# Kernel optimization log

Hardware: AMD Instinct MI355X
Metric: run time of the kernel (lower is better)

The kernel has to match this reference:

```python
import jax, jax.numpy as jnp
import numpy as np

N_NODES = 100000
N_EDGES = 1600000
NODE_DIM = 128
HIDDEN_DIM = 128


def _sage_conv(x, src, dst, deg_inv, W_l, W_r, b):
    # PyG SAGEConv (aggr='mean', root_weight=True):
    #   out = lin_l(mean_{j in N(i)} x_j) + lin_r(x_i)
    msgs = x[src]                                             # [E, d_in] gather
    agg = jax.ops.segment_sum(msgs, dst, num_segments=N_NODES)  # [N, d_in]
    mean = agg * deg_inv[:, None]
    return mean @ W_l + x @ W_r + b


def setup_inputs() -> dict:
    key = jax.random.key(0)
    ks = jax.random.split(key, 9)
    x = jax.random.normal(ks[0], (N_NODES, NODE_DIM), dtype=jnp.float32)
    edge_index = jax.random.randint(ks[1], (2, N_EDGES), 0, N_NODES, dtype=jnp.int32)
    t = jnp.zeros((1,), dtype=jnp.float32)

    def glorot(k, fan_in, fan_out):
        s = (6.0 / (fan_in + fan_out)) ** 0.5
        return jax.random.uniform(k, (fan_in, fan_out), jnp.float32, -s, s)

    return {
        "t": t,
        "x": x,
        "edge_index": edge_index,
        "W1_l": glorot(ks[2], NODE_DIM, HIDDEN_DIM),
        "W1_r": glorot(ks[3], NODE_DIM, HIDDEN_DIM),
        "b1": jnp.zeros((HIDDEN_DIM,), jnp.float32),
        "W2_l": glorot(ks[4], HIDDEN_DIM, HIDDEN_DIM),
        "W2_r": glorot(ks[5], HIDDEN_DIM, HIDDEN_DIM),
        "b2": jnp.zeros((HIDDEN_DIM,), jnp.float32),
        "W3_l": glorot(ks[6], HIDDEN_DIM, NODE_DIM),
        "W3_r": glorot(ks[7], HIDDEN_DIM, NODE_DIM),
        "b3": jnp.zeros((NODE_DIM,), jnp.float32),
    }


def reference(t, x, edge_index, W1_l, W1_r, b1, W2_l, W2_r, b2, W3_l, W3_r, b3):
    src, dst = edge_index[0], edge_index[1]
    deg = jax.ops.segment_sum(jnp.ones((N_EDGES,), x.dtype), dst, num_segments=N_NODES)
    deg_inv = jnp.where(deg > 0, 1.0 / jnp.maximum(deg, 1.0), 0.0)

    h = jax.nn.relu(_sage_conv(x, src, dst, deg_inv, W1_l, W1_r, b1))
    h = jax.nn.relu(_sage_conv(h, src, dst, deg_inv, W2_l, W2_r, b2))
    dx_dt = _sage_conv(h, src, dst, deg_inv, W3_l, W3_r, b3)
    return dx_dt
```

## Files before the change

kernel.cpp:

```cpp
#include <hip/hip_runtime.h>

#define NN   100000
#define NE   1600000
#define DIM  128
#define NBKT 391
#define EPB  4096
#define NBLK 391
#define NTILES (NN / 16)
#define CASTB 12500
#define CWB   384


typedef short          s16x8 __attribute__((ext_vector_type(8)));
typedef unsigned short u16x8 __attribute__((ext_vector_type(8)));
typedef float          f32x4 __attribute__((ext_vector_type(4)));

__device__ __forceinline__ unsigned short f2b(float f) {
    unsigned u = __float_as_uint(f);
    unsigned r = ((u >> 16) & 1u) + 0x7FFFu;
    return (unsigned short)((u + r) >> 16);
}
__device__ __forceinline__ float b2f(unsigned short h) {
    return __uint_as_float(((unsigned)h) << 16);
}

__global__ void k_prep(const float* __restrict__ x, unsigned short* __restrict__ xb,
                       const int* __restrict__ dst, int* __restrict__ hist,
                       const float* __restrict__ W1l, const float* __restrict__ W1r,
                       const float* __restrict__ W2l, const float* __restrict__ W2r,
                       const float* __restrict__ W3l, const float* __restrict__ W3r,
                       unsigned short* __restrict__ Wt1, unsigned short* __restrict__ Wt2,
                       unsigned short* __restrict__ Wt3) {
    __shared__ int lh[NBKT];
    int t = threadIdx.x, b = blockIdx.x;
    if (b < NBLK) {
        for (int j = t; j < NBKT; j += 256) lh[j] = 0;
        __syncthreads();
        int base = b * EPB;
        int end = base + EPB; if (end > NE) end = NE;
        for (int i = base + t; i < end; i += 256) atomicAdd(&lh[dst[i] >> 8], 1);
        __syncthreads();
        for (int j = t; j < NBKT; j += 256) hist[j * NBLK + b] = lh[j];
    } else if (b < NBLK + CASTB) {
        int i = (b - NBLK) * 256 + t;
        float4 v = ((const float4*)x)[i];
        ushort4 o;
        o.x = f2b(v.x); o.y = f2b(v.y); o.z = f2b(v.z); o.w = f2b(v.w);
        ((ushort4*)xb)[i] = o;
    } else {
        int i = (b - NBLK - CASTB) * 256 + t;
        int L = i >> 15;
        int rem = i & 32767;
        int n = rem >> 8;
        int k = rem & 255;
        const float* Wl = (L == 0) ? W1l : (L == 1) ? W2l : W3l;
        const float* Wr = (L == 0) ? W1r : (L == 1) ? W2r : W3r;
        unsigned short* Wt = (L == 0) ? Wt1 : (L == 1) ? Wt2 : Wt3;
        float v = (k < 128) ? Wl[k * 128 + n] : Wr[(k - 128) * 128 + n];
        Wt[n * 256 + k] = f2b(v);
    }
}

__global__ void k_scanrow(int* __restrict__ hist, int* __restrict__ row_total) {
    __shared__ int sh[512];
    int k = blockIdx.x, t = threadIdx.x;
    int v = (t < NBLK) ? hist[k * NBLK + t] : 0;
    sh[t] = v;
    __syncthreads();
    for (int off = 1; off < 512; off <<= 1) {
        int a = (t >= off) ? sh[t - off] : 0;
        __syncthreads();
        sh[t] += a;
        __syncthreads();
    }
    if (t < NBLK) hist[k * NBLK + t] = sh[t] - v;
    if (t == 511) row_total[k] = sh[511];
}

__global__ void k_bin2(const int* __restrict__ src, const int* __restrict__ dst,
                       const int* __restrict__ hist, const int* __restrict__ row_total,
                       int* __restrict__ bbase, int* __restrict__ binned) {
    __shared__ int s_base[NBKT];
    __shared__ int s_cnt[NBKT];
    __shared__ int ps[256];
    int t = threadIdx.x, b = blockIdx.x;
    int a0 = (2 * t     < NBKT) ? row_total[2 * t]     : 0;
    int a1 = (2 * t + 1 < NBKT) ? row_total[2 * t + 1] : 0;
    ps[t] = a0 + a1;
    __syncthreads();
    for (int off = 1; off < 256; off <<= 1) {
        int v = (t >= off) ? ps[t - off] : 0;
        __syncthreads();
        ps[t] += v;
        __syncthreads();
    }
    int pe = ps[t] - (a0 + a1);
    if (2 * t     < NBKT) s_base[2 * t]     = pe;
    if (2 * t + 1 < NBKT) s_base[2 * t + 1] = pe + a0;
    __syncthreads();
    if (b == 0) {
        for (int j = t; j < NBKT; j += 256) bbase[j] = s_base[j];
        if (t == 0) bbase[NBKT] = NE;
    }
    for (int j = t; j < NBKT; j += 256) {
        s_base[j] += hist[j * NBLK + b];
        s_cnt[j] = 0;
    }
    __syncthreads();
    int base = b * EPB;
    int end = base + EPB; if (end > NE) end = NE;
    for (int i = base + t; i < end; i += 256) {
        int d = dst[i];
        int k = d >> 8;
        int w = (src[i] << 8) | (d & 255);
        int lpos = atomicAdd(&s_cnt[k], 1);
        binned[s_base[k] + lpos] = w;
    }
}

__global__ void k_build(const int* __restrict__ binned,
                        const int* __restrict__ bucket_base,
                        int* __restrict__ csr, int4* __restrict__ meta) {
    __shared__ int s_deg[256], s_scan[256], s_cur[256];
    __shared__ int stage[8192];
    int b = blockIdx.x, t = threadIdx.x;
    int base = bucket_base[b], end = bucket_base[b + 1];
    int cnt = end - base;
    s_deg[t] = 0;
    __syncthreads();
    for (int i = t; i < cnt; i += 256)
        atomicAdd(&s_deg[binned[base + i] & 255], 1);
    __syncthreads();
    s_scan[t] = s_deg[t];
    __syncthreads();
    for (int off = 1; off < 256; off <<= 1) {
        int a = (t >= off) ? s_scan[t - off] : 0;
        __syncthreads();
        s_scan[t] += a;
        __syncthreads();
    }
    int excl = s_scan[t] - s_deg[t];
    s_cur[t] = excl;
    int node = b * 256 + t;
    if (node < NN) {
        int d = s_deg[t];
        float di = (d > 0) ? 1.0f / (float)d : 0.0f;
        int4 M; M.x = base + excl; M.y = d; M.z = __float_as_int(di); M.w = 0;
        meta[node] = M;
    }
    __syncthreads();
    for (int i = t; i < cnt; i += 256) {
        int w = binned[base + i];
        int pos = atomicAdd(&s_cur[w & 255], 1);
        int s = w >> 8;
        if (pos < 8192) stage[pos] = s;
        else            csr[base + pos] = s;
    }
    __syncthreads();
    int m = cnt < 8192 ? cnt : 8192;
    for (int i = t; i < m; i += 256) csr[base + i] = stage[i];
}

__global__ void k_gather(const unsigned short* __restrict__ feat,
                         const int4* __restrict__ meta,
                         const int* __restrict__ csr,
                         unsigned short* __restrict__ mean) {
    int lane = threadIdx.x & 63;
    int wv   = threadIdx.x >> 6;
    int n    = blockIdx.x * 4 + wv;
    int q = lane >> 4, c = lane & 15;
    int4 M = meta[n];
    int base = M.x;
    int d    = M.y;
    float s  = __int_as_float(M.z);
    float acc0[8], acc1[8];
#pragma unroll
    for (int t = 0; t < 8; t++) { acc0[t] = 0.0f; acc1[t] = 0.0f; }
    const u16x8* fp = (const u16x8*)feat;
    int j = q;
    for (; j + 4 < d; j += 8) {
        int s0 = csr[base + j];
        int s1 = csr[base + j + 4];
        u16x8 v0 = fp[s0 * 16 + c];
        u16x8 v1 = fp[s1 * 16 + c];
#pragma unroll
        for (int t = 0; t < 8; t++) { acc0[t] += b2f(v0[t]); acc1[t] += b2f(v1[t]); }
    }
    if (j < d) {
        int s0 = csr[base + j];
        u16x8 v0 = fp[s0 * 16 + c];
#pragma unroll
        for (int t = 0; t < 8; t++) acc0[t] += b2f(v0[t]);
    }
#pragma unroll
    for (int t = 0; t < 8; t++) acc0[t] += acc1[t];
#pragma unroll
    for (int t = 0; t < 8; t++) {
        acc0[t] += __shfl_xor(acc0[t], 16, 64);
        acc0[t] += __shfl_xor(acc0[t], 32, 64);
    }
    if (q == 0) {
        u16x8 o;
#pragma unroll
        for (int t = 0; t < 8; t++) o[t] = f2b(acc0[t] * s);
        ((u16x8*)mean)[n * 16 + c] = o;
    }
}

template <int MODE>
__global__ void __launch_bounds__(512)
k_lin(const unsigned short* __restrict__ meanb,
      const unsigned short* __restrict__ hb,
      const unsigned short* __restrict__ Wt,
      const float* __restrict__ bias, void* __restrict__ out) {
    __shared__ s16x8 sW[4096];
    int t = threadIdx.x;
    const s16x8* wp = (const s16x8*)Wt;
#pragma unroll
    for (int it = 0; it < 8; it++) {
        int ci = it * 512 + t;
        int frag = ci >> 6, ln = ci & 63;
        int mt = frag >> 3, kt = frag & 7;
        int m = mt * 16 + (ln & 15);
        int kc = kt * 4 + (ln >> 4);
        sW[ci] = wp[m * 32 + kc];
    }
    __syncthreads();

    int lane = t & 63;
    int wv   = t >> 6;
    int tile = blockIdx.x * 8 + wv;
    if (tile >= NTILES) return;
    int n0 = tile * 16;
    int q = lane >> 4, c = lane & 15;
    const s16x8* mp = (const s16x8*)meanb;
    const s16x8* hp = (const s16x8*)hb;
    int row = n0 + c;
    s16x8 B[8];
#pragma unroll
    for (int kt = 0; kt < 4; kt++) B[kt] = mp[row * 16 + kt * 4 + q];
#pragma unroll
    for (int kt = 0; kt < 4; kt++) B[4 + kt] = hp[row * 16 + kt * 4 + q];
    const f32x4* bp = (const f32x4*)bias;
#pragma unroll
    for (int mt = 0; mt < 8; mt++) {
        f32x4 acc = {0.f, 0.f, 0.f, 0.f};
#pragma unroll
        for (int kt = 0; kt < 8; kt++)
            acc = __builtin_amdgcn_mfma_f32_16x16x32_bf16(sW[(mt * 8 + kt) * 64 + lane],
                                                          B[kt], acc, 0, 0, 0);
        f32x4 bv = bp[mt * 4 + q];
        int node = n0 + c;
        if (MODE == 0) {
            ushort4 o;
            float v0 = acc[0] + bv[0]; if (v0 < 0.f) v0 = 0.f;
            float v1 = acc[1] + bv[1]; if (v1 < 0.f) v1 = 0.f;
            float v2 = acc[2] + bv[2]; if (v2 < 0.f) v2 = 0.f;
            float v3 = acc[3] + bv[3]; if (v3 < 0.f) v3 = 0.f;
            o.x = f2b(v0); o.y = f2b(v1); o.z = f2b(v2); o.w = f2b(v3);
            ((ushort4*)out)[node * 32 + mt * 4 + q] = o;
        } else {
            f32x4 v;
#pragma unroll
            for (int r = 0; r < 4; r++) v[r] = acc[r] + bv[r];
            ((f32x4*)out)[node * 32 + mt * 4 + q] = v;
        }
    }
}

extern "C" void kernel_launch(void* const* d_in, const int* in_sizes, int n_in,
                              void* d_out, int out_size, void* d_ws, size_t ws_size,
                              hipStream_t stream) {
    const float* x   = (const float*)d_in[1];
    const int*   ei  = (const int*)d_in[2];
    const int*   src = ei;
    const int*   dst = ei + NE;
    const float* W1l = (const float*)d_in[3];
    const float* W1r = (const float*)d_in[4];
    const float* b1  = (const float*)d_in[5];
    const float* W2l = (const float*)d_in[6];
    const float* W2r = (const float*)d_in[7];
    const float* b2  = (const float*)d_in[8];
    const float* W3l = (const float*)d_in[9];
    const float* W3r = (const float*)d_in[10];
    const float* b3  = (const float*)d_in[11];

    char* w = (char*)d_ws;
    auto carve = [&](size_t bytes) {
        void* p = (void*)w;
        w += (bytes + 255) & ~(size_t)255;
        return p;
    };
    int4*  meta      = (int4*)carve((size_t)NN * 16);
    int*   hist      = (int*)carve((size_t)NBKT * NBLK * 4);
    int*   row_total = (int*)carve(NBKT * 4);
    int*   bbase     = (int*)carve((NBKT + 1) * 4);
    int*   csr       = (int*)carve((size_t)NE * 4);
    unsigned short* Wt1 = (unsigned short*)carve(128 * 256 * 2);
    unsigned short* Wt2 = (unsigned short*)carve(128 * 256 * 2);
    unsigned short* Wt3 = (unsigned short*)carve(128 * 256 * 2);
    unsigned short* xb    = (unsigned short*)carve((size_t)NN * DIM * 2);
    unsigned short* meanb = (unsigned short*)carve((size_t)NN * DIM * 2);
    unsigned short* h1b   = (unsigned short*)carve((size_t)NN * DIM * 2);
    unsigned short* h2b   = xb;
    int*   binned    = (int*)meanb;

    k_prep<<<NBLK + CASTB + CWB, 256, 0, stream>>>(x, xb, dst, hist,
                                                   W1l, W1r, W2l, W2r, W3l, W3r,
                                                   Wt1, Wt2, Wt3);
    k_scanrow<<<NBKT, 512, 0, stream>>>(hist, row_total);
    k_bin2<<<NBLK, 256, 0, stream>>>(src, dst, hist, row_total, bbase, binned);
    k_build<<<NBKT, 256, 0, stream>>>(binned, bbase, csr, meta);

    const int GB = NN / 4;
    const int LB = (NTILES + 7) / 8;

    k_gather<<<GB, 256, 0, stream>>>(xb, meta, csr, meanb);
    k_lin<0><<<LB, 512, 0, stream>>>(meanb, xb, Wt1, b1, (void*)h1b);
    k_gather<<<GB, 256, 0, stream>>>(h1b, meta, csr, meanb);
    k_lin<0><<<LB, 512, 0, stream>>>(meanb, h1b, Wt2, b2, (void*)h2b);
    k_gather<<<GB, 256, 0, stream>>>(h2b, meta, csr, meanb);
    k_lin<1><<<LB, 512, 0, stream>>>(meanb, h2b, Wt3, b3, d_out);
}
```

Before: 417.9 us.

## Replace bucketed CSR build with atomic degree count and scatter; enlarge linear blocks

The two-level bucket histogram, scan, bin and per-bucket build pipeline is replaced by three simple kernels. One counts per-node degree with global atomics, one computes row offsets with a per-block redundant prefix sum, and one scatters sources into CSR via atomic cursors. The bf16 cast now handles two float4 per thread, and the linear kernel uses 1024-thread blocks with activation loads issued before the weight staging. The simpler build drops several launches and passes, but global atomics on contended destinations, a quadratic-ish prefix sum in k_meta, and non-deterministic neighbour order within each row (so float summation order varies) are the trade-offs.

```diff
diff --git a/kernel.cpp b/kernel.cpp
--- a/kernel.cpp
+++ b/kernel.cpp
@@ -3,12 +3,13 @@
 #define NN   100000
 #define NE   1600000
 #define DIM  128
-#define NBKT 391
-#define EPB  4096
-#define NBLK 391
+#define ZB    391
+#define CASTB 6250
+#define CWB   384
+#define EB    6250
 #define NTILES (NN / 16)
-#define CASTB 12500
-#define CWB   384
+#define LB    ((NTILES + 15) / 16)
+#define GB    (NN / 4)
 
 
 typedef short          s16x8 __attribute__((ext_vector_type(8)));
@@ -25,30 +26,27 @@
 }
 
 __global__ void k_prep(const float* __restrict__ x, unsigned short* __restrict__ xb,
-                       const int* __restrict__ dst, int* __restrict__ hist,
+                       int* __restrict__ deg,
                        const float* __restrict__ W1l, const float* __restrict__ W1r,
                        const float* __restrict__ W2l, const float* __restrict__ W2r,
                        const float* __restrict__ W3l, const float* __restrict__ W3r,
                        unsigned short* __restrict__ Wt1, unsigned short* __restrict__ Wt2,
                        unsigned short* __restrict__ Wt3) {
-    __shared__ int lh[NBKT];
     int t = threadIdx.x, b = blockIdx.x;
-    if (b < NBLK) {
-        for (int j = t; j < NBKT; j += 256) lh[j] = 0;
-        __syncthreads();
-        int base = b * EPB;
-        int end = base + EPB; if (end > NE) end = NE;
-        for (int i = base + t; i < end; i += 256) atomicAdd(&lh[dst[i] >> 8], 1);
-        __syncthreads();
-        for (int j = t; j < NBKT; j += 256) hist[j * NBLK + b] = lh[j];
-    } else if (b < NBLK + CASTB) {
-        int i = (b - NBLK) * 256 + t;
-        float4 v = ((const float4*)x)[i];
-        ushort4 o;
-        o.x = f2b(v.x); o.y = f2b(v.y); o.z = f2b(v.z); o.w = f2b(v.w);
-        ((ushort4*)xb)[i] = o;
+    if (b < ZB) {
+        int n = b * 256 + t;
+        if (n < NN) deg[n] = 0;
+    } else if (b < ZB + CASTB) {
+        int i0 = (b - ZB) * 512 + t;
+        float4 v0 = ((const float4*)x)[i0];
+        float4 v1 = ((const float4*)x)[i0 + 256];
+        ushort4 o0, o1;
+        o0.x = f2b(v0.x); o0.y = f2b(v0.y); o0.z = f2b(v0.z); o0.w = f2b(v0.w);
+        o1.x = f2b(v1.x); o1.y = f2b(v1.y); o1.z = f2b(v1.z); o1.w = f2b(v1.w);
+        ((ushort4*)xb)[i0]       = o0;
+        ((ushort4*)xb)[i0 + 256] = o1;
     } else {
-        int i = (b - NBLK - CASTB) * 256 + t;
+        int i = (b - ZB - CASTB) * 256 + t;
         int L = i >> 15;
         int rem = i & 32767;
         int n = rem >> 8;
@@ -61,104 +59,52 @@
     }
 }
 
-__global__ void k_scanrow(int* __restrict__ hist, int* __restrict__ row_total) {
-    __shared__ int sh[512];
-    int k = blockIdx.x, t = threadIdx.x;
-    int v = (t < NBLK) ? hist[k * NBLK + t] : 0;
-    sh[t] = v;
-    __syncthreads();
-    for (int off = 1; off < 512; off <<= 1) {
-        int a = (t >= off) ? sh[t - off] : 0;
-        __syncthreads();
-        sh[t] += a;
-        __syncthreads();
-    }
-    if (t < NBLK) hist[k * NBLK + t] = sh[t] - v;
-    if (t == 511) row_total[k] = sh[511];
-}
-
-__global__ void k_bin2(const int* __restrict__ src, const int* __restrict__ dst,
-                       const int* __restrict__ hist, const int* __restrict__ row_total,
-                       int* __restrict__ bbase, int* __restrict__ binned) {
-    __shared__ int s_base[NBKT];
-    __shared__ int s_cnt[NBKT];
+__global__ void k_degcnt(const int* __restrict__ dst, int* __restrict__ deg) {
+    int i = blockIdx.x * 256 + threadIdx.x;
+    atomicAdd(&deg[dst[i]], 1);
+}
+
+__global__ void k_meta(const int* __restrict__ deg, int4* __restrict__ meta,
+                       int* __restrict__ cursor) {
     __shared__ int ps[256];
     int t = threadIdx.x, b = blockIdx.x;
-    int a0 = (2 * t     < NBKT) ? row_total[2 * t]     : 0;
-    int a1 = (2 * t + 1 < NBKT) ? row_total[2 * t + 1] : 0;
-    ps[t] = a0 + a1;
+    int start = b * 256;
+    int partial = 0;
+    for (int i = t; i < start; i += 256) partial += deg[i];
+    ps[t] = partial;
+    __syncthreads();
+    for (int off = 128; off > 0; off >>= 1) {
+        if (t < off) ps[t] += ps[t + off];
+        __syncthreads();
+    }
+    int S = ps[0];
+    __syncthreads();
+    int n = start + t;
+    int d = (n < NN) ? deg[n] : 0;
+    ps[t] = d;
     __syncthreads();
     for (int off = 1; off < 256; off <<= 1) {
-        int v = (t >= off) ? ps[t - off] : 0;
+        int a = (t >= off) ? ps[t - off] : 0;
         __syncthreads();
-        ps[t] += v;
+        ps[t] += a;
         __syncthreads();
     }
-    int pe = ps[t] - (a0 + a1);
-    if (2 * t     < NBKT) s_base[2 * t]     = pe;
-    if (2 * t + 1 < NBKT) s_base[2 * t + 1] = pe + a0;
-    __syncthreads();
-    if (b == 0) {
-        for (int j = t; j < NBKT; j += 256) bbase[j] = s_base[j];
-        if (t == 0) bbase[NBKT] = NE;
-    }
-    for (int j = t; j < NBKT; j += 256) {
-        s_base[j] += hist[j * NBLK + b];
-        s_cnt[j] = 0;
-    }
-    __syncthreads();
-    int base = b * EPB;
-    int end = base + EPB; if (end > NE) end = NE;
-    for (int i = base + t; i < end; i += 256) {
-        int d = dst[i];
-        int k = d >> 8;
-        int w = (src[i] << 8) | (d & 255);
-        int lpos = atomicAdd(&s_cnt[k], 1);
-        binned[s_base[k] + lpos] = w;
-    }
-}
-
-__global__ void k_build(const int* __restrict__ binned,
-                        const int* __restrict__ bucket_base,
-                        int* __restrict__ csr, int4* __restrict__ meta) {
-    __shared__ int s_deg[256], s_scan[256], s_cur[256];
-    __shared__ int stage[8192];
-    int b = blockIdx.x, t = threadIdx.x;
-    int base = bucket_base[b], end = bucket_base[b + 1];
-    int cnt = end - base;
-    s_deg[t] = 0;
-    __syncthreads();
-    for (int i = t; i < cnt; i += 256)
-        atomicAdd(&s_deg[binned[base + i] & 255], 1);
-    __syncthreads();
-    s_scan[t] = s_deg[t];
-    __syncthreads();
-    for (int off = 1; off < 256; off <<= 1) {
-        int a = (t >= off) ? s_scan[t - off] : 0;
-        __syncthreads();
-        s_scan[t] += a;
-        __syncthreads();
-    }
-    int excl = s_scan[t] - s_deg[t];
-    s_cur[t] = excl;
-    int node = b * 256 + t;
-    if (node < NN) {
-        int d = s_deg[t];
+    int rs = S + (ps[t] - d);
+    if (n < NN) {
         float di = (d > 0) ? 1.0f / (float)d : 0.0f;
-        int4 M; M.x = base + excl; M.y = d; M.z = __float_as_int(di); M.w = 0;
-        meta[node] = M;
-    }
-    __syncthreads();
-    for (int i = t; i < cnt; i += 256) {
-        int w = binned[base + i];
-        int pos = atomicAdd(&s_cur[w & 255], 1);
-        int s = w >> 8;
-        if (pos < 8192) stage[pos] = s;
-        else            csr[base + pos] = s;
-    }
-    __syncthreads();
-    int m = cnt < 8192 ? cnt : 8192;
-    for (int i = t; i < m; i += 256) csr[base + i] = stage[i];
+        int4 M; M.x = rs; M.y = d; M.z = __float_as_int(di); M.w = 0;
+        meta[n]   = M;
+        cursor[n] = rs;
+    }
+}
+
+__global__ void k_scatter(const int* __restrict__ src, const int* __restrict__ dst,
+                          int* __restrict__ cursor, int* __restrict__ csr) {
+    int i = blockIdx.x * 256 + threadIdx.x;
+    int s  = src[i];
+    int d_ = dst[i];
+    int pos = atomicAdd(&cursor[d_], 1);
+    csr[pos] = s;
 }
 
 __global__ void k_gather(const unsigned short* __restrict__ feat,
@@ -208,17 +154,33 @@
 }
 
 template <int MODE>
-__global__ void __launch_bounds__(512)
+__global__ void __launch_bounds__(1024)
 k_lin(const unsigned short* __restrict__ meanb,
       const unsigned short* __restrict__ hb,
       const unsigned short* __restrict__ Wt,
       const float* __restrict__ bias, void* __restrict__ out) {
     __shared__ s16x8 sW[4096];
     int t = threadIdx.x;
+    int lane = t & 63;
+    int wv   = t >> 6;
+    int tile = blockIdx.x * 16 + wv;
+    bool act = (tile < NTILES);
+    int n0 = tile * 16;
+    int q = lane >> 4, c = lane & 15;
+    int row = n0 + c;
+    s16x8 B[8];
+    if (act) {
+        const s16x8* mp = (const s16x8*)meanb;
+        const s16x8* hp = (const s16x8*)hb;
+#pragma unroll
+        for (int kt = 0; kt < 4; kt++) B[kt] = mp[row * 16 + kt * 4 + q];
+#pragma unroll
+        for (int kt = 0; kt < 4; kt++) B[4 + kt] = hp[row * 16 + kt * 4 + q];
+    }
     const s16x8* wp = (const s16x8*)Wt;
 #pragma unroll
-    for (int it = 0; it < 8; it++) {
-        int ci = it * 512 + t;
+    for (int it = 0; it < 4; it++) {
+        int ci = it * 1024 + t;
         int frag = ci >> 6, ln = ci & 63;
         int mt = frag >> 3, kt = frag & 7;
         int m = mt * 16 + (ln & 15);
@@ -226,21 +188,8 @@
         sW[ci] = wp[m * 32 + kc];
     }
     __syncthreads();
-
-    int lane = t & 63;
-    int wv   = t >> 6;
-    int tile = blockIdx.x * 8 + wv;
-    if (tile >= NTILES) return;
-    int n0 = tile * 16;
-    int q = lane >> 4, c = lane & 15;
-    const s16x8* mp = (const s16x8*)meanb;
-    const s16x8* hp = (const s16x8*)hb;
-    int row = n0 + c;
-    s16x8 B[8];
-#pragma unroll
-    for (int kt = 0; kt < 4; kt++) B[kt] = mp[row * 16 + kt * 4 + q];
-#pragma unroll
-    for (int kt = 0; kt < 4; kt++) B[4 + kt] = hp[row * 16 + kt * 4 + q];
+    if (!act) return;
+
     const f32x4* bp = (const f32x4*)bias;
 #pragma unroll
     for (int mt = 0; mt < 8; mt++) {
@@ -291,11 +240,10 @@
         w += (bytes + 255) & ~(size_t)255;
         return p;
     };
-    int4*  meta      = (int4*)carve((size_t)NN * 16);
-    int*   hist      = (int*)carve((size_t)NBKT * NBLK * 4);
-    int*   row_total = (int*)carve(NBKT * 4);
-    int*   bbase     = (int*)carve((NBKT + 1) * 4);
-    int*   csr       = (int*)carve((size_t)NE * 4);
+    int4*  meta    = (int4*)carve((size_t)NN * 16);
+    int*   deg     = (int*)carve((size_t)NN * 4);
+    int*   cursor  = (int*)carve((size_t)NN * 4);
+    int*   csr     = (int*)carve((size_t)NE * 4);
     unsigned short* Wt1 = (unsigned short*)carve(128 * 256 * 2);
     unsigned short* Wt2 = (unsigned short*)carve(128 * 256 * 2);
     unsigned short* Wt3 = (unsigned short*)carve(128 * 256 * 2);
@@ -303,22 +251,18 @@
     unsigned short* meanb = (unsigned short*)carve((size_t)NN * DIM * 2);
     unsigned short* h1b   = (unsigned short*)carve((size_t)NN * DIM * 2);
     unsigned short* h2b   = xb;
-    int*   binned    = (int*)meanb;
-
-    k_prep<<<NBLK + CASTB + CWB, 256, 0, stream>>>(x, xb, dst, hist,
-                                                   W1l, W1r, W2l, W2r, W3l, W3r,
-                                                   Wt1, Wt2, Wt3);
-    k_scanrow<<<NBKT, 512, 0, stream>>>(hist, row_total);
-    k_bin2<<<NBLK, 256, 0, stream>>>(src, dst, hist, row_total, bbase, binned);
-    k_build<<<NBKT, 256, 0, stream>>>(binned, bbase, csr, meta);
-
-    const int GB = NN / 4;
-    const int LB = (NTILES + 7) / 8;
+
+    k_prep<<<ZB + CASTB + CWB, 256, 0, stream>>>(x, xb, deg,
+                                                 W1l, W1r, W2l, W2r, W3l, W3r,
+                                                 Wt1, Wt2, Wt3);
+    k_degcnt<<<EB, 256, 0, stream>>>(dst, deg);
+    k_meta<<<ZB, 256, 0, stream>>>(deg, meta, cursor);
+    k_scatter<<<EB, 256, 0, stream>>>(src, dst, cursor, csr);
 
     k_gather<<<GB, 256, 0, stream>>>(xb, meta, csr, meanb);
-    k_lin<0><<<LB, 512, 0, stream>>>(meanb, xb, Wt1, b1, (void*)h1b);
+    k_lin<0><<<LB, 1024, 0, stream>>>(meanb, xb, Wt1, b1, (void*)h1b);
     k_gather<<<GB, 256, 0, stream>>>(h1b, meta, csr, meanb);
-    k_lin<0><<<LB, 512, 0, stream>>>(meanb, h1b, Wt2, b2, (void*)h2b);
+    k_lin<0><<<LB, 1024, 0, stream>>>(meanb, h1b, Wt2, b2, (void*)h2b);
     k_gather<<<GB, 256, 0, stream>>>(h2b, meta, csr, meanb);
-    k_lin<1><<<LB, 512, 0, stream>>>(meanb, h2b, Wt3, b3, d_out);
-}
+    k_lin<1><<<LB, 1024, 0, stream>>>(meanb, h2b, Wt3, b3, d_out);
+}
```

Result: slower. 610.2 us (+46.0%).
